# Kernel optimization log

Measured on AMD Instinct MI355X. Metric: run time of the kernel, lower is better.

## Reference

```python
import jax, jax.numpy as jnp
import numpy as np

B, N, H, L, R, E = 8, 10000, 64, 4, 3, 200000
FP, NUM_CELLS = 2048, 100
LN_EPS = 1e-3  # Keras LayerNormalization default epsilon


def setup_inputs() -> dict:
    key = jax.random.key(0)
    ks = jax.random.split(key, 24)
    g = lambda k, shape, fan: (jax.random.uniform(k, shape, jnp.float32) * 2 - 1) * np.sqrt(6.0 / fan)
    inp = {
        'ctl_expr': jax.random.normal(ks[0], (B, N), jnp.float32),
        'drug_targets': jax.random.uniform(ks[1], (B, N), jnp.float32),
        'drug_fp': jax.random.uniform(ks[2], (B, FP), jnp.float32),
        'edge_weight': jax.random.uniform(ks[3], (R, E), jnp.float32),
        'cell_idx': jax.random.randint(ks[4], (B,), 0, NUM_CELLS, jnp.int32),
        'edge_index': jax.random.randint(ks[5], (R, 2, E), 0, N, jnp.int32),
        # parameters
        'W_se': g(ks[6], (1, H), 1 + H),
        'b_se': jnp.zeros((H,), jnp.float32),
        'cell_emb': jax.random.normal(ks[7], (NUM_CELLS, H), jnp.float32) * 0.05,
        'W_f1': g(ks[8], (FP, H), FP + H),
        'b_f1': jnp.zeros((H,), jnp.float32),
        'W_f2': g(ks[9], (H, 2 * H), 3 * H) * 0.1,
        'b_f2': jnp.zeros((2 * H,), jnp.float32),
        'Wself': jnp.stack([g(ks[10 + l], (H, H), 2 * H) for l in range(L)]),
        'Wrel': jnp.stack([jnp.stack([g(jax.random.fold_in(ks[14], l * R + r), (H, H), 2 * H) for r in range(R)]) for l in range(L)]),
        'ln_g': jnp.ones((L, H), jnp.float32),
        'ln_b': jnp.zeros((L, H), jnp.float32),
        'W_out': g(ks[15], (H, 1), H + 1),
        'b_out': jnp.zeros((1,), jnp.float32),
    }
    return inp


def reference(ctl_expr, drug_targets, drug_fp, edge_weight, cell_idx, edge_index,
              W_se, b_se, cell_emb, W_f1, b_f1, W_f2, b_f2,
              Wself, Wrel, ln_g, ln_b, W_out, b_out):
    # shared_embedding: Dense(H, relu) applied to scalar node features
    def shared(v):  # v: [B,N] -> [B,N,H]
        return jax.nn.relu(v[..., None] * W_se[0] + b_se)

    x = shared(ctl_expr) + shared(drug_targets)            # [B,N,H]
    x = x + cell_emb[cell_idx][:, None, :]                 # cell embedding broadcast

    # drug FiLM: gamma/beta conditioning
    film = jax.nn.relu(drug_fp @ W_f1 + b_f1) @ W_f2 + b_f2  # [B,2H]
    gamma, beta = jnp.split(film, 2, axis=-1)
    gamma = jnp.tanh(gamma)
    x = x * (1.0 + gamma[:, None, :]) + beta[:, None, :]

    n_layers, n_rel = Wself.shape[0], Wrel.shape[1]
    for l in range(n_layers):
        out = x @ Wself[l]                                 # self projection [B,N,H]
        for r in range(n_rel):
            src, dst = edge_index[r, 0], edge_index[r, 1]
            h = x @ Wrel[l, r]                             # [B,N,H]
            msg = edge_weight[r][None, :, None] * h[:, src, :]  # [B,E,H]
            out = out.at[:, dst].add(msg)                  # scatter-add to dst nodes
        # LayerNorm over feature dim (Keras eps=1e-3)
        mu = out.mean(-1, keepdims=True)
        var = ((out - mu) ** 2).mean(-1, keepdims=True)
        out = (out - mu) * jax.lax.rsqrt(var + LN_EPS) * ln_g[l] + ln_b[l]
        x = jax.nn.relu(out)

    return (x @ W_out)[..., 0] + b_out[0]                  # [B,N]
```

## Files before the change

kernel.cpp:

```cpp
#include <hip/hip_runtime.h>
#include <hip/hip_bf16.h>
#include <math.h>

#define Bk 8
#define Nk 10000
#define Hk 64
#define Lk 4
#define Rk 3
#define Ek 200000
#define FPk 2048

#define C4 (Rk*Ek/4)
#define CNT4B ((C4 + 255)/256)
#define INITB 2048

typedef unsigned short u16;
typedef unsigned int   u32;
typedef _Float16 f16;
typedef __attribute__((ext_vector_type(2))) _Float16 f16x2;
typedef __attribute__((ext_vector_type(8))) _Float16 f16x8;
typedef __attribute__((ext_vector_type(4))) float f32x4;

__device__ __forceinline__ f16x2 as_h2(u32 u){
    union{u32 i; f16x2 h;} v; v.i = u; return v.h;
}
__device__ __forceinline__ u32 as_u32(f16x2 h){
    union{u32 i; f16x2 h;} v; v.h = h; return v.i;
}
__device__ __forceinline__ u16 f2h_bits(float f){
    union{f16 h; u16 u;} v; v.h = (f16)f; return v.u;
}

__global__ void k_prep0(const float* __restrict__ Wself, const float* __restrict__ Wrel,
                        u16* __restrict__ wt, int* __restrict__ deg,
                        const float* __restrict__ fp, const float* __restrict__ W1,
                        const float* __restrict__ b1, float* __restrict__ hid){
    __shared__ float red[256];
    if(blockIdx.x < 256){
        int idx = blockIdx.x*256 + threadIdx.x;
        if(idx < Rk*Nk) deg[idx] = 0;
        int j    = idx & 7;
        int lane = (idx >> 3) & 63;
        int jt   = (idx >> 9) & 3;
        int kc   = (idx >> 11) & 1;
        int mt   = (idx >> 12) & 3;
        int l    = idx >> 14;
        int k    = kc*32 + (lane >> 4)*8 + j;
        int col  = jt*16 + (lane & 15);
        float w = (mt == 0) ? Wself[(l*64 + k)*64 + col]
                            : Wrel[((l*3 + (mt-1))*64 + k)*64 + col];
        wt[idx] = f2h_bits(w);
    }else{
        int bb = blockIdx.x - 256;
        int b = bb >> 6, h = bb & 63;
        const float* fpb = fp + b*FPk;
        float acc = 0.f;
        for(int k = threadIdx.x; k < FPk; k += 256)
            acc += fpb[k] * W1[k*64 + h];
        red[threadIdx.x] = acc;
        __syncthreads();
        for(int s = 128; s >= 1; s >>= 1){
            if(threadIdx.x < s) red[threadIdx.x] += red[threadIdx.x + s];
            __syncthreads();
        }
        if(threadIdx.x == 0) hid[b*64 + h] = fmaxf(red[0] + b1[h], 0.f);
    }
}

__global__ void k_fill2(const int* __restrict__ edge_index, const float* __restrict__ edge_weight,
                        int* __restrict__ deg, int2* __restrict__ epack,
                        const float* __restrict__ ctl, const float* __restrict__ dt,
                        const int* __restrict__ cell_idx,
                        const float* __restrict__ W_se, const float* __restrict__ b_se,
                        const float* __restrict__ cell_emb,
                        const float* __restrict__ hid, const float* __restrict__ W2,
                        const float* __restrict__ b2,
                        u16* __restrict__ xh){
    __shared__ float g1l[64], btl[64];
    if(blockIdx.x < CNT4B){
        int idx = blockIdx.x*256 + threadIdx.x;
        if(idx >= C4) return;
        int g = idx*4;
        int r = g / Ek, e = g % Ek;
        int4   s4 = *(const int4*)  &edge_index [r*2*Ek + e];
        int4   d4 = *(const int4*)  &edge_index [r*2*Ek + Ek + e];
        float4 w4 = *(const float4*)&edge_weight[r*Ek + e];
        int* dg = deg + r*Nk;
        size_t ebase = (size_t)r*Nk;
        int pos; f16 h;
        pos = atomicAdd(&dg[d4.x], 1); h = (f16)w4.x;
        if(pos < 64) epack[((ebase + d4.x) << 6) + pos] = make_int2(s4.x << 7, (int)as_u32((f16x2){h, h}));
        pos = atomicAdd(&dg[d4.y], 1); h = (f16)w4.y;
        if(pos < 64) epack[((ebase + d4.y) << 6) + pos] = make_int2(s4.y << 7, (int)as_u32((f16x2){h, h}));
        pos = atomicAdd(&dg[d4.z], 1); h = (f16)w4.z;
        if(pos < 64) epack[((ebase + d4.z) << 6) + pos] = make_int2(s4.z << 7, (int)as_u32((f16x2){h, h}));
        pos = atomicAdd(&dg[d4.w], 1); h = (f16)w4.w;
        if(pos < 64) epack[((ebase + d4.w) << 6) + pos] = make_int2(s4.w << 7, (int)as_u32((f16x2){h, h}));
    }else{
        int bb  = blockIdx.x - CNT4B;
        int b   = bb >> 8;
        int blk = bb & 255;
        int t = threadIdx.x;
        if(t < 128){
            float acc = b2[t];
            #pragma unroll 8
            for(int k = 0; k < 64; ++k)
                acc += hid[b*64 + k] * W2[k*128 + t];
            if(t < 64) g1l[t] = 1.f + tanhf(acc);
            else       btl[t - 64] = acc;
        }
        __syncthreads();
        int ci = cell_idx[b];
        const int per_b = Nk*8;
        for(int o = blk*256 + t; o < per_b; o += 256*256){
            int hq = o & 7;
            int n  = o >> 3;
            float c = ctl[b*Nk + n], d = dt[b*Nk + n];
            u32 pk[4];
            #pragma unroll
            for(int j = 0; j < 8; j += 2){
                int h0 = hq*8 + j, h1 = h0 + 1;
                float w0 = W_se[h0], s0 = b_se[h0];
                float w1 = W_se[h1], s1 = b_se[h1];
                float v0 = fmaxf(c*w0 + s0, 0.f) + fmaxf(d*w0 + s0, 0.f)
                         + cell_emb[ci*64 + h0];
                float v1 = fmaxf(c*w1 + s1, 0.f) + fmaxf(d*w1 + s1, 0.f)
                         + cell_emb[ci*64 + h1];
                v0 = v0 * g1l[h0] + btl[h0];
                v1 = v1 * g1l[h1] + btl[h1];
                pk[j >> 1] = (u32)f2h_bits(v0) | ((u32)f2h_bits(v1) << 16);
            }
            *(int4*)&xh[(((size_t)b*Nk + n)*64) + hq*8] = make_int4(pk[0], pk[1], pk[2], pk[3]);
        }
    }
}

__global__ __launch_bounds__(256) void k_agg(const u16* __restrict__ xh,
                      const int* __restrict__ deg, const int2* __restrict__ epack,
                      u16* __restrict__ aggh){
    __shared__ int2 stash[4][64];
    int bpair = blockIdx.x & 3;
    int grp   = blockIdx.x >> 2;
    int wq    = threadIdx.x >> 6;
    int wid   = grp*4 + wq;
    int lane  = threadIdx.x & 63;
    int fg    = lane & 31;
    int bl    = lane >> 5;
    int b     = bpair*2 + bl;
    int r = wid / Nk, dst = wid % Nk;
    int cnt = deg[wid]; if(cnt > 64) cnt = 64;
    const int2* ep = epack + ((size_t)wid << 6);
    const char* xb = (const char*)xh + (size_t)b*Nk*128 + fg*4;

    f16x2 A = (f16x2){0,0}, C = (f16x2){0,0};
    int2* st = stash[wq];
    if(lane < cnt) st[lane] = ep[lane];
    int t = 0;
    for(; t + 8 <= cnt; t += 8){
        int4 q01 = *(const int4*)&st[t];
        int4 q23 = *(const int4*)&st[t+2];
        int4 q45 = *(const int4*)&st[t+4];
        int4 q67 = *(const int4*)&st[t+6];
        u32 u0 = *(const u32*)(xb + q01.x);
        u32 u1 = *(const u32*)(xb + q01.z);
        u32 u2 = *(const u32*)(xb + q23.x);
        u32 u3 = *(const u32*)(xb + q23.z);
        u32 u4 = *(const u32*)(xb + q45.x);
        u32 u5 = *(const u32*)(xb + q45.z);
        u32 u6 = *(const u32*)(xb + q67.x);
        u32 u7 = *(const u32*)(xb + q67.z);
        A += as_h2(u0)*as_h2(q01.y); C += as_h2(u1)*as_h2(q01.w);
        A += as_h2(u2)*as_h2(q23.y); C += as_h2(u3)*as_h2(q23.w);
        A += as_h2(u4)*as_h2(q45.y); C += as_h2(u5)*as_h2(q45.w);
        A += as_h2(u6)*as_h2(q67.y); C += as_h2(u7)*as_h2(q67.w);
    }
    for(; t + 2 <= cnt; t += 2){
        int4 q01 = *(const int4*)&st[t];
        u32 u0 = *(const u32*)(xb + q01.x);
        u32 u1 = *(const u32*)(xb + q01.z);
        A += as_h2(u0)*as_h2(q01.y); C += as_h2(u1)*as_h2(q01.w);
    }
    if(t < cnt){
        int2 p = st[t];
        u32 u = *(const u32*)(xb + p.x);
        A += as_h2(u)*as_h2(p.y);
    }
    float a0 = (float)A.x + (float)C.x;
    float a1 = (float)A.y + (float)C.y;
    u32 packed = (u32)f2h_bits(a0) | ((u32)f2h_bits(a1) << 16);
    ((u32*)aggh)[(((size_t)r*Bk + b)*Nk + dst)*32 + fg] = packed;
}

__global__ __launch_bounds__(256) void k_proj_mfma(u16* __restrict__ xh,
        const u16* __restrict__ aggh, const u16* __restrict__ wt,
        const float* __restrict__ ln_g, const float* __restrict__ ln_b, int l,
        int last, const float* __restrict__ W_out, const float* __restrict__ b_out,
        float* __restrict__ out){
    __shared__ u16 wls[16384];
    const u16* wl = wt + (size_t)l*16384;
    for(int i = threadIdx.x; i < 2048; i += 256)
        *(int4*)&wls[i*8] = *(const int4*)&wl[i*8];
    __syncthreads();

    int lane = threadIdx.x & 63;
    int wq   = threadIdx.x >> 6;
    int k8   = blockIdx.x & 7;
    int b    = ((k8 & 3) << 1) | (k8 >> 2);
    int tile = blockIdx.x >> 3;
    int n0   = tile*128 + wq*32;
    int mrow = lane & 15;
    int kq   = lane >> 4;
    int nA = n0 + mrow;       if(nA >= Nk) nA = Nk - 1;
    int nB = n0 + 16 + mrow;  if(nB >= Nk) nB = Nk - 1;

    f32x4 accA[4], accB[4];
    #pragma unroll
    for(int jt = 0; jt < 4; ++jt){
        accA[jt] = (f32x4){0.f,0.f,0.f,0.f};
        accB[jt] = (f32x4){0.f,0.f,0.f,0.f};
    }

    #pragma unroll
    for(int mt = 0; mt < 4; ++mt){
        const u16* basep = (mt == 0)
            ? xh   + (size_t)b*Nk*64
            : aggh + (((size_t)(mt-1)*Bk + b)*Nk)*64;
        const u16* arowA = basep + (size_t)nA*64;
        const u16* arowB = basep + (size_t)nB*64;
        #pragma unroll
        for(int kc = 0; kc < 2; ++kc){
            f16x8 aA = *(const f16x8*)(arowA + kc*32 + kq*8);
            f16x8 aB = *(const f16x8*)(arowB + kc*32 + kq*8);
            #pragma unroll
            for(int jt = 0; jt < 4; ++jt){
                f16x8 bfrag = *(const f16x8*)(wls + ((size_t)((mt*2 + kc)*4 + jt)*64 + lane)*8);
                accA[jt] = __builtin_amdgcn_mfma_f32_16x16x32_f16(aA, bfrag, accA[jt], 0, 0, 0);
                accB[jt] = __builtin_amdgcn_mfma_f32_16x16x32_f16(aB, bfrag, accB[jt], 0, 0, 0);
            }
        }
    }

    float gv[4], bv[4], wo[4];
    #pragma unroll
    for(int jt = 0; jt < 4; ++jt){
        int f = jt*16 + mrow;
        gv[jt] = ln_g[l*64 + f];
        bv[jt] = ln_b[l*64 + f];
        wo[jt] = W_out[f];
    }
    float bo = b_out[0];
    u16* xdst = xh + (size_t)b*Nk*64;

    #pragma unroll
    for(int half = 0; half < 2; ++half){
        f32x4* acc = half ? accB : accA;
        int nbase = n0 + half*16;
        #pragma unroll
        for(int v = 0; v < 4; ++v){
            float s1 = acc[0][v] + acc[1][v] + acc[2][v] + acc[3][v];
            float s2 = acc[0][v]*acc[0][v] + acc[1][v]*acc[1][v]
                     + acc[2][v]*acc[2][v] + acc[3][v]*acc[3][v];
            #pragma unroll
            for(int off = 1; off <= 8; off <<= 1){
                s1 += __shfl_xor(s1, off);
                s2 += __shfl_xor(s2, off);
            }
            float mu  = s1 * 0.015625f;
            float var = s2 * 0.015625f - mu*mu;
            float rstd = rsqrtf(var + 1e-3f);
            int node = nbase + kq*4 + v;
            if(!last){
                if(node < Nk){
                    #pragma unroll
                    for(int jt = 0; jt < 4; ++jt){
                        float o = (acc[jt][v] - mu) * rstd * gv[jt] + bv[jt];
                        xdst[(size_t)node*64 + jt*16 + mrow] = f2h_bits(fmaxf(o, 0.f));
                    }
                }
            }else{
                float s3 = 0.f;
                #pragma unroll
                for(int jt = 0; jt < 4; ++jt){
                    float o = (acc[jt][v] - mu) * rstd * gv[jt] + bv[jt];
                    s3 += fmaxf(o, 0.f) * wo[jt];
                }
                #pragma unroll
                for(int off = 1; off <= 8; off <<= 1)
                    s3 += __shfl_xor(s3, off);
                if(mrow == 0 && node < Nk)
                    out[(size_t)b*Nk + node] = s3 + bo;
            }
        }
    }
}

extern "C" void kernel_launch(void* const* d_in, const int* in_sizes, int n_in,
                              void* d_out, int out_size, void* d_ws, size_t ws_size,
                              hipStream_t stream){
    const float* ctl        = (const float*)d_in[0];
    const float* dt         = (const float*)d_in[1];
    const float* drug_fp    = (const float*)d_in[2];
    const float* edge_w     = (const float*)d_in[3];
    const int*   cell_idx   = (const int*)  d_in[4];
    const int*   edge_index = (const int*)  d_in[5];
    const float* W_se       = (const float*)d_in[6];
    const float* b_se       = (const float*)d_in[7];
    const float* cell_emb   = (const float*)d_in[8];
    const float* W_f1       = (const float*)d_in[9];
    const float* b_f1       = (const float*)d_in[10];
    const float* W_f2       = (const float*)d_in[11];
    const float* b_f2       = (const float*)d_in[12];
    const float* Wself      = (const float*)d_in[13];
    const float* Wrel       = (const float*)d_in[14];
    const float* ln_g       = (const float*)d_in[15];
    const float* ln_b       = (const float*)d_in[16];
    const float* W_out      = (const float*)d_in[17];
    const float* b_out      = (const float*)d_in[18];
    float* out = (float*)d_out;

    char* p = (char*)d_ws;
    auto alloc = [&](size_t bytes)->char*{
        char* r = p; p += (bytes + 255) & ~(size_t)255; return r;
    };
    int*   deg    = (int*)  alloc((size_t)Rk*Nk*4);
    int2*  epack  = (int2*) alloc((size_t)Rk*Nk*64*8);
    float* hid    = (float*)alloc((size_t)Bk*64*4);
    u16*   xh     = (u16*)  alloc((size_t)Bk*Nk*64*2);
    u16*   aggh   = (u16*)  alloc((size_t)3*Bk*Nk*64*2);
    u16*   wt     = (u16*)  alloc((size_t)Lk*16384*2);

    k_prep0<<<256 + Bk*64, 256, 0, stream>>>(Wself, Wrel, wt, deg,
                                             drug_fp, W_f1, b_f1, hid);
    k_fill2<<<CNT4B + INITB, 256, 0, stream>>>(edge_index, edge_w, deg, epack,
                                               ctl, dt, cell_idx, W_se, b_se, cell_emb,
                                               hid, W_f2, b_f2, xh);

    const int ntile = (Nk + 127)/128;
    for(int l = 0; l < Lk; ++l){
        k_agg<<<4*7500, 256, 0, stream>>>(xh, deg, epack, aggh);
        k_proj_mfma<<<ntile*8, 256, 0, stream>>>(
            xh, aggh, wt, ln_g, ln_b, l,
            (l == Lk-1) ? 1 : 0, W_out, b_out, out);
    }
}
```

Baseline: 374.4 us.

## Pad degree counters, compact edge records, split fill kernel from x init

The per-destination degree counters are padded to one per 64-byte stride so atomics on different nodes stop contending on the same cache line. Edge records shrink from 8 to 4 bytes, packing a 16-bit source index with a half-precision weight, and are expanded into the old LDS stash format inside the aggregation kernel. The combined fill/init kernel is split into two launches. The trade-offs are a larger zero-initialised degree buffer, extra unpacking work in every aggregation call, and one more kernel launch.

```diff
diff --git a/kernel.cpp b/kernel.cpp
--- a/kernel.cpp
+++ b/kernel.cpp
@@ -13,6 +13,7 @@
 #define C4 (Rk*Ek/4)
 #define CNT4B ((C4 + 255)/256)
 #define INITB 2048
+#define DEGW  (Rk*Nk*16)
 
 typedef unsigned short u16;
 typedef unsigned int   u32;
@@ -38,7 +39,10 @@
     __shared__ float red[256];
     if(blockIdx.x < 256){
         int idx = blockIdx.x*256 + threadIdx.x;
-        if(idx < Rk*Nk) deg[idx] = 0;
+        if(idx < DEGW/8){
+            *(int4*)&deg[idx*8]     = make_int4(0,0,0,0);
+            *(int4*)&deg[idx*8 + 4] = make_int4(0,0,0,0);
+        }
         int j    = idx & 7;
         int lane = (idx >> 3) & 63;
         int jt   = (idx >> 9) & 3;
@@ -67,9 +71,29 @@
     }
 }
 
-__global__ void k_fill2(const int* __restrict__ edge_index, const float* __restrict__ edge_weight,
-                        int* __restrict__ deg, int2* __restrict__ epack,
-                        const float* __restrict__ ctl, const float* __restrict__ dt,
+__global__ void k_efill(const int* __restrict__ edge_index, const float* __restrict__ edge_weight,
+                        int* __restrict__ deg, u32* __restrict__ epack){
+    int idx = blockIdx.x*256 + threadIdx.x;
+    if(idx >= C4) return;
+    int g = idx*4;
+    int r = g / Ek, e = g % Ek;
+    int4   s4 = *(const int4*)  &edge_index [r*2*Ek + e];
+    int4   d4 = *(const int4*)  &edge_index [r*2*Ek + Ek + e];
+    float4 w4 = *(const float4*)&edge_weight[r*Ek + e];
+    int* dg = deg + (size_t)r*Nk*16;
+    size_t ebase = (size_t)r*Nk;
+    int pos;
+    pos = atomicAdd(&dg[(size_t)d4.x*16], 1);
+    if(pos < 64) epack[((ebase + d4.x) << 6) + pos] = ((u32)f2h_bits(w4.x) << 16) | (u32)s4.x;
+    pos = atomicAdd(&dg[(size_t)d4.y*16], 1);
+    if(pos < 64) epack[((ebase + d4.y) << 6) + pos] = ((u32)f2h_bits(w4.y) << 16) | (u32)s4.y;
+    pos = atomicAdd(&dg[(size_t)d4.z*16], 1);
+    if(pos < 64) epack[((ebase + d4.z) << 6) + pos] = ((u32)f2h_bits(w4.z) << 16) | (u32)s4.z;
+    pos = atomicAdd(&dg[(size_t)d4.w*16], 1);
+    if(pos < 64) epack[((ebase + d4.w) << 6) + pos] = ((u32)f2h_bits(w4.w) << 16) | (u32)s4.w;
+}
+
+__global__ void k_xinit(const float* __restrict__ ctl, const float* __restrict__ dt,
                         const int* __restrict__ cell_idx,
                         const float* __restrict__ W_se, const float* __restrict__ b_se,
                         const float* __restrict__ cell_emb,
@@ -77,66 +101,44 @@
                         const float* __restrict__ b2,
                         u16* __restrict__ xh){
     __shared__ float g1l[64], btl[64];
-    if(blockIdx.x < CNT4B){
-        int idx = blockIdx.x*256 + threadIdx.x;
-        if(idx >= C4) return;
-        int g = idx*4;
-        int r = g / Ek, e = g % Ek;
-        int4   s4 = *(const int4*)  &edge_index [r*2*Ek + e];
-        int4   d4 = *(const int4*)  &edge_index [r*2*Ek + Ek + e];
-        float4 w4 = *(const float4*)&edge_weight[r*Ek + e];
-        int* dg = deg + r*Nk;
-        size_t ebase = (size_t)r*Nk;
-        int pos; f16 h;
-        pos = atomicAdd(&dg[d4.x], 1); h = (f16)w4.x;
-        if(pos < 64) epack[((ebase + d4.x) << 6) + pos] = make_int2(s4.x << 7, (int)as_u32((f16x2){h, h}));
-        pos = atomicAdd(&dg[d4.y], 1); h = (f16)w4.y;
-        if(pos < 64) epack[((ebase + d4.y) << 6) + pos] = make_int2(s4.y << 7, (int)as_u32((f16x2){h, h}));
-        pos = atomicAdd(&dg[d4.z], 1); h = (f16)w4.z;
-        if(pos < 64) epack[((ebase + d4.z) << 6) + pos] = make_int2(s4.z << 7, (int)as_u32((f16x2){h, h}));
-        pos = atomicAdd(&dg[d4.w], 1); h = (f16)w4.w;
-        if(pos < 64) epack[((ebase + d4.w) << 6) + pos] = make_int2(s4.w << 7, (int)as_u32((f16x2){h, h}));
-    }else{
-        int bb  = blockIdx.x - CNT4B;
-        int b   = bb >> 8;
-        int blk = bb & 255;
-        int t = threadIdx.x;
-        if(t < 128){
-            float acc = b2[t];
-            #pragma unroll 8
-            for(int k = 0; k < 64; ++k)
-                acc += hid[b*64 + k] * W2[k*128 + t];
-            if(t < 64) g1l[t] = 1.f + tanhf(acc);
-            else       btl[t - 64] = acc;
-        }
-        __syncthreads();
-        int ci = cell_idx[b];
-        const int per_b = Nk*8;
-        for(int o = blk*256 + t; o < per_b; o += 256*256){
-            int hq = o & 7;
-            int n  = o >> 3;
-            float c = ctl[b*Nk + n], d = dt[b*Nk + n];
-            u32 pk[4];
-            #pragma unroll
-            for(int j = 0; j < 8; j += 2){
-                int h0 = hq*8 + j, h1 = h0 + 1;
-                float w0 = W_se[h0], s0 = b_se[h0];
-                float w1 = W_se[h1], s1 = b_se[h1];
-                float v0 = fmaxf(c*w0 + s0, 0.f) + fmaxf(d*w0 + s0, 0.f)
-                         + cell_emb[ci*64 + h0];
-                float v1 = fmaxf(c*w1 + s1, 0.f) + fmaxf(d*w1 + s1, 0.f)
-                         + cell_emb[ci*64 + h1];
-                v0 = v0 * g1l[h0] + btl[h0];
-                v1 = v1 * g1l[h1] + btl[h1];
-                pk[j >> 1] = (u32)f2h_bits(v0) | ((u32)f2h_bits(v1) << 16);
-            }
-            *(int4*)&xh[(((size_t)b*Nk + n)*64) + hq*8] = make_int4(pk[0], pk[1], pk[2], pk[3]);
-        }
+    int b   = blockIdx.x >> 8;
+    int blk = blockIdx.x & 255;
+    int t = threadIdx.x;
+    if(t < 128){
+        float acc = b2[t];
+        #pragma unroll 8
+        for(int k = 0; k < 64; ++k)
+            acc += hid[b*64 + k] * W2[k*128 + t];
+        if(t < 64) g1l[t] = 1.f + tanhf(acc);
+        else       btl[t - 64] = acc;
+    }
+    __syncthreads();
+    int ci = cell_idx[b];
+    const int per_b = Nk*8;
+    for(int o = blk*256 + t; o < per_b; o += 256*256){
+        int hq = o & 7;
+        int n  = o >> 3;
+        float c = ctl[b*Nk + n], d = dt[b*Nk + n];
+        u32 pk[4];
+        #pragma unroll
+        for(int j = 0; j < 8; j += 2){
+            int h0 = hq*8 + j, h1 = h0 + 1;
+            float w0 = W_se[h0], s0 = b_se[h0];
+            float w1 = W_se[h1], s1 = b_se[h1];
+            float v0 = fmaxf(c*w0 + s0, 0.f) + fmaxf(d*w0 + s0, 0.f)
+                     + cell_emb[ci*64 + h0];
+            float v1 = fmaxf(c*w1 + s1, 0.f) + fmaxf(d*w1 + s1, 0.f)
+                     + cell_emb[ci*64 + h1];
+            v0 = v0 * g1l[h0] + btl[h0];
+            v1 = v1 * g1l[h1] + btl[h1];
+            pk[j >> 1] = (u32)f2h_bits(v0) | ((u32)f2h_bits(v1) << 16);
+        }
+        *(int4*)&xh[(((size_t)b*Nk + n)*64) + hq*8] = make_int4(pk[0], pk[1], pk[2], pk[3]);
     }
 }
 
 __global__ __launch_bounds__(256) void k_agg(const u16* __restrict__ xh,
-                      const int* __restrict__ deg, const int2* __restrict__ epack,
+                      const int* __restrict__ deg, const u32* __restrict__ epack,
                       u16* __restrict__ aggh){
     __shared__ int2 stash[4][64];
     int bpair = blockIdx.x & 3;
@@ -148,13 +150,17 @@
     int bl    = lane >> 5;
     int b     = bpair*2 + bl;
     int r = wid / Nk, dst = wid % Nk;
-    int cnt = deg[wid]; if(cnt > 64) cnt = 64;
-    const int2* ep = epack + ((size_t)wid << 6);
+    int cnt = deg[(size_t)wid*16]; if(cnt > 64) cnt = 64;
+    const u32* ep = epack + ((size_t)wid << 6);
     const char* xb = (const char*)xh + (size_t)b*Nk*128 + fg*4;
 
     f16x2 A = (f16x2){0,0}, C = (f16x2){0,0};
     int2* st = stash[wq];
-    if(lane < cnt) st[lane] = ep[lane];
+    if(lane < cnt){
+        u32 e = ep[lane];
+        st[lane] = make_int2((int)((e & 0xFFFFu) << 7),
+                             (int)((e >> 16) | (e & 0xFFFF0000u)));
+    }
     int t = 0;
     for(; t + 8 <= cnt; t += 8){
         int4 q01 = *(const int4*)&st[t];
@@ -322,8 +328,8 @@
     auto alloc = [&](size_t bytes)->char*{
         char* r = p; p += (bytes + 255) & ~(size_t)255; return r;
     };
-    int*   deg    = (int*)  alloc((size_t)Rk*Nk*4);
-    int2*  epack  = (int2*) alloc((size_t)Rk*Nk*64*8);
+    int*   deg    = (int*)  alloc((size_t)DEGW*4);
+    u32*   epack  = (u32*)  alloc((size_t)Rk*Nk*64*4);
     float* hid    = (float*)alloc((size_t)Bk*64*4);
     u16*   xh     = (u16*)  alloc((size_t)Bk*Nk*64*2);
     u16*   aggh   = (u16*)  alloc((size_t)3*Bk*Nk*64*2);
@@ -331,9 +337,9 @@
 
     k_prep0<<<256 + Bk*64, 256, 0, stream>>>(Wself, Wrel, wt, deg,
                                              drug_fp, W_f1, b_f1, hid);
-    k_fill2<<<CNT4B + INITB, 256, 0, stream>>>(edge_index, edge_w, deg, epack,
-                                               ctl, dt, cell_idx, W_se, b_se, cell_emb,
-                                               hid, W_f2, b_f2, xh);
+    k_efill<<<CNT4B, 256, 0, stream>>>(edge_index, edge_w, deg, epack);
+    k_xinit<<<INITB, 256, 0, stream>>>(ctl, dt, cell_idx, W_se, b_se, cell_emb,
+                                       hid, W_f2, b_f2, xh);
 
     const int ntile = (Nk + 127)/128;
     for(int l = 0; l < Lk; ++l){
```

New measurement: 362.6 us. -3.2%, faster.
